# Performance work log

Hardware: AMD Instinct MI355X
Metric: run time of the kernel (lower is better)

Reference implementation:

```python
import jax, jax.numpy as jnp
import numpy as np

N_NODES = 50000
N_EDGES = 800000
D = 128


def setup_inputs() -> dict:
    key = jax.random.key(0)
    ks = jax.random.split(key, 5)
    x = jax.random.normal(ks[0], (N_NODES, D), dtype=jnp.float32)
    edge_index = jax.random.randint(ks[1], (2, N_EDGES), 0, N_NODES, dtype=jnp.int64)
    # GCNConv linear weight + bias, and the two DGCN parameters
    Wc = jax.random.normal(ks[2], (D, D), dtype=jnp.float32) / np.sqrt(D)
    bc = jnp.zeros((D,), dtype=jnp.float32)
    W0 = jax.random.normal(ks[3], (D, D), dtype=jnp.float32)
    Wt = jax.random.normal(ks[4], (D, D), dtype=jnp.float32)
    return {"x": x, "edge_index": edge_index, "Wc": Wc, "bc": bc, "W0": W0, "Wt": Wt}


def gcn_conv(x, edge_index, Wc, bc):
    # PyG GCNConv: add self-loops, symmetric normalization D^-1/2 (A+I) D^-1/2,
    # applied to x @ Wc, plus bias.
    n = x.shape[0]
    loops = jnp.arange(n, dtype=edge_index.dtype)
    src = jnp.concatenate([edge_index[0], loops])  # [E+N]
    dst = jnp.concatenate([edge_index[1], loops])
    ones = jnp.ones(src.shape[0], dtype=x.dtype)
    deg = jax.ops.segment_sum(ones, dst, num_segments=n)  # in-degree incl. self-loop
    dinv = jnp.where(deg > 0, jax.lax.rsqrt(deg), 0.0)
    norm = dinv[src] * dinv[dst]  # [E+N]
    xw = x @ Wc  # [N, D]
    msgs = xw[src] * norm[:, None]  # gather + scale  [E+N, D]
    agg = jax.ops.segment_sum(msgs, dst, num_segments=n)  # scatter-add  [N, D]
    return agg + bc


def reference(x, edge_index, Wc, bc, W0, Wt):
    h_neigh = gcn_conv(x, edge_index, Wc, bc)
    h_self = x @ W0
    h_change = (h_neigh - x) @ Wt
    return h_neigh + h_self + h_change
```

## Files before the change

### kernel.cpp

```cpp
#include <hip/hip_runtime.h>

#define N_NODES 50000
#define N_EDGES 800000
#define D 128
#define NB 196
#define CAPB 8192
#define P1_BLOCKS 256
#define EPB ((N_EDGES + P1_BLOCKS - 1) / P1_BLOCKS)
#define CAP 64

typedef __attribute__((ext_vector_type(8))) short short8;
typedef __attribute__((ext_vector_type(4))) float f32x4;

__device__ __forceinline__ unsigned short f2bf(float f) {
    unsigned int u = __builtin_bit_cast(unsigned int, f);
    u += 0x7FFFu + ((u >> 16) & 1u);
    return (unsigned short)(u >> 16);
}
__device__ __forceinline__ float bf2f(unsigned short h) {
    unsigned int u = ((unsigned int)h) << 16;
    return __builtin_bit_cast(float, u);
}

__global__ void k_init(int* __restrict__ gcur) {
    const int t = threadIdx.x;
    if (t < NB) gcur[t] = t * CAPB;
}

__global__ __launch_bounds__(256) void k_part1(const int* __restrict__ src,
                                               const int* __restrict__ dst,
                                               int* __restrict__ gcur,
                                               unsigned int* __restrict__ pbuf) {
    __shared__ unsigned int stage[NB][CAP + 1];
    __shared__ int scnt[NB];
    const int t = threadIdx.x;
    for (int i = t; i < NB; i += 256) scnt[i] = 0;
    __syncthreads();

    const long e0 = (long)blockIdx.x * EPB;
    const long e1 = (e0 + EPB < N_EDGES) ? e0 + EPB : N_EDGES;
    for (long e = e0 + t; e < e1; e += 256) {
        const int s = src[e];
        const int d = dst[e];
        const int b = d >> 8;
        const unsigned int p = ((unsigned int)(d & 255) << 16) | (unsigned int)s;
        const int slot = atomicAdd(&scnt[b], 1);
        if (slot < CAP) {
            stage[b][slot] = p;
        } else {
            const int pos = atomicAdd(&gcur[b], 1);
            pbuf[pos] = p;
        }
    }
    __syncthreads();
    if (t < NB) {
        const int n = (scnt[t] < CAP) ? scnt[t] : CAP;
        if (n > 0) {
            const int pos = atomicAdd(&gcur[t], n);
            for (int i = 0; i < n; ++i) pbuf[pos + i] = stage[t][i];
        }
    }
}

__global__ __launch_bounds__(256) void k_part2(const unsigned int* __restrict__ pbuf,
                                               const int* __restrict__ gcur,
                                               int* __restrict__ row_start,
                                               int* __restrict__ cnt,
                                               float* __restrict__ dinv,
                                               int* __restrict__ esrc) {
    __shared__ int lcnt[256];
    __shared__ int lcur[256];
    __shared__ int stmp[256];
    const int b = blockIdx.x;
    const int t = threadIdx.x;
    const int base = b * CAPB;
    const int n = gcur[b] - base;

    lcnt[t] = 0;
    __syncthreads();
    for (int i = t; i < n; i += 256) atomicAdd(&lcnt[pbuf[base + i] >> 16], 1);
    __syncthreads();

    const int c = lcnt[t];
    stmp[t] = c;
    __syncthreads();
    for (int off = 1; off < 256; off <<= 1) {
        int u = (t >= off) ? stmp[t - off] : 0;
        __syncthreads();
        stmp[t] += u;
        __syncthreads();
    }
    const int ls = base + stmp[t] - c;
    lcur[t] = ls;
    const int node = b * 256 + t;
    if (node < N_NODES) {
        row_start[node] = ls;
        cnt[node] = c;
        dinv[node] = rsqrtf((float)c + 1.0f);
    }
    __syncthreads();

    for (int i = t; i < n; i += 256) {
        const unsigned int p = pbuf[base + i];
        const int pos = atomicAdd(&lcur[p >> 16], 1);
        esrc[pos] = (int)(p & 0xFFFFu);
    }
}

__global__ __launch_bounds__(256) void k_wx(const float* __restrict__ Wc,
                                            const float* __restrict__ W0,
                                            const float* __restrict__ Wt,
                                            const float* __restrict__ bc,
                                            const float* __restrict__ x,
                                            const float* __restrict__ dinv,
                                            unsigned short* __restrict__ Wp,
                                            float* __restrict__ bv,
                                            unsigned short* __restrict__ xd,
                                            unsigned short* __restrict__ gx) {
    __shared__ float sWt[D * D];
    const int t = threadIdx.x;

    if (blockIdx.x < 17) {
        for (int i = t * 4; i < D * D; i += 256 * 4)
            *(float4*)(sWt + i) = *(const float4*)(Wt + i);
        __syncthreads();

        if (blockIdx.x == 16) {
            if (t < D) {
                float acc = bc[t];
#pragma unroll 16
                for (int k = 0; k < D; ++k) acc += bc[k] * sWt[k * D + t];
                bv[t] = acc;
            }
            return;
        }
        const int id = blockIdx.x * 256 + t;
        const int lane = id & 63;
        const int tile = (id >> 6) & 7;
        const int step = id >> 9;
        const int n = tile * 16 + (lane & 15);
        const int kbase = step * 32 + (lane >> 4) * 8;
        unsigned short v[8];
#pragma unroll
        for (int j = 0; j < 8; ++j) {
            const int k = kbase + j;
            float f;
            if (k < D) {
                f = Wc[k * D + n];
#pragma unroll 16
                for (int m = 0; m < D; ++m) f += Wc[k * D + m] * sWt[m * D + n];
            } else {
                f = W0[(k - D) * D + n] - sWt[(k - D) * D + n];
            }
            v[j] = f2bf(f);
        }
        *(uint4*)(Wp + (long)id * 8) = *(uint4*)v;
        return;
    }

    const int gid = (blockIdx.x - 17) * 256 + t;
    const int node = gid >> 4;
    const int c = gid & 15;
    const float di = dinv[node];
    const float4 a = ((const float4*)x)[(long)node * 32 + c * 2];
    const float4 b = ((const float4*)x)[(long)node * 32 + c * 2 + 1];
    const float f[8] = {a.x, a.y, a.z, a.w, b.x, b.y, b.z, b.w};
    unsigned short vd[8], vb[8];
#pragma unroll
    for (int j = 0; j < 8; ++j) {
        vd[j] = f2bf(di * f[j]);
        vb[j] = f2bf(f[j]);
    }
    *(uint4*)(xd + (long)node * 128 + c * 8) = *(uint4*)vd;
    *(uint4*)(gx + (long)node * 256 + 128 + c * 8) = *(uint4*)vb;
}

__global__ __launch_bounds__(256) void k_gather(const unsigned short* __restrict__ xd,
                                                const int* __restrict__ row_start,
                                                const int* __restrict__ cnt,
                                                const int* __restrict__ esrc,
                                                const float* __restrict__ dinv,
                                                unsigned short* __restrict__ gx) {
    const int node = blockIdx.x * 4 + (threadIdx.x >> 6);
    const int lane = threadIdx.x & 63;
    const int c = lane & 15;
    const int s = lane >> 4;
    const int begin = row_start[node];
    const int end = begin + cnt[node];

    float acc[8] = {};
    int i = begin + s;
    for (; i + 12 < end; i += 16) {
        const int a0 = esrc[i];
        const int a1 = esrc[i + 4];
        const int a2 = esrc[i + 8];
        const int a3 = esrc[i + 12];
        const short8 v0 = *(const short8*)(xd + (long)a0 * 128 + c * 8);
        const short8 v1 = *(const short8*)(xd + (long)a1 * 128 + c * 8);
        const short8 v2 = *(const short8*)(xd + (long)a2 * 128 + c * 8);
        const short8 v3 = *(const short8*)(xd + (long)a3 * 128 + c * 8);
#pragma unroll
        for (int j = 0; j < 8; ++j)
            acc[j] += (bf2f((unsigned short)v0[j]) + bf2f((unsigned short)v1[j])) +
                      (bf2f((unsigned short)v2[j]) + bf2f((unsigned short)v3[j]));
    }
    for (; i < end; i += 4) {
        const int a0 = esrc[i];
        const short8 v0 = *(const short8*)(xd + (long)a0 * 128 + c * 8);
#pragma unroll
        for (int j = 0; j < 8; ++j) acc[j] += bf2f((unsigned short)v0[j]);
    }

#pragma unroll
    for (int j = 0; j < 8; ++j) {
        acc[j] += __shfl_xor(acc[j], 16);
        acc[j] += __shfl_xor(acc[j], 32);
    }

    if (s == 0) {
        const float di = dinv[node];
        const short8 xs = *(const short8*)(xd + (long)node * 128 + c * 8);
        unsigned short o[8];
#pragma unroll
        for (int j = 0; j < 8; ++j)
            o[j] = f2bf(di * (acc[j] + bf2f((unsigned short)xs[j])));
        *(uint4*)(gx + (long)node * 256 + c * 8) = *(uint4*)o;
    }
}

__global__ __launch_bounds__(256) void k_mm(const unsigned short* __restrict__ gx,
                                            const unsigned short* __restrict__ Wp,
                                            const float* __restrict__ bv,
                                            float* __restrict__ out) {
    const int tid = threadIdx.x;
    const int wave = tid >> 6;
    const int lane = tid & 63;
    const int quad = lane >> 4;
    const int lr = lane & 15;
    const int row0 = blockIdx.x * 64 + wave * 16;

    int ar = row0 + lr;
    if (ar >= N_NODES) ar = N_NODES - 1;
    const unsigned short* aptr = gx + (long)ar * 256 + quad * 8;

    f32x4 acc[8] = {};

#pragma unroll
    for (int s = 0; s < 8; ++s) {
        const short8 a = *(const short8*)(aptr + s * 32);
#pragma unroll
        for (int t = 0; t < 8; ++t) {
            const short8 b = *(const short8*)(Wp + ((long)(s * 8 + t) * 64 + lane) * 8);
            acc[t] = __builtin_amdgcn_mfma_f32_16x16x32_bf16(a, b, acc[t], 0, 0, 0);
        }
    }

#pragma unroll
    for (int t = 0; t < 8; ++t) {
        const int col = t * 16 + lr;
        const float bvv = bv[col];
#pragma unroll
        for (int r = 0; r < 4; ++r) {
            const int row = row0 + quad * 4 + r;
            if (row < N_NODES) out[(long)row * D + col] = acc[t][r] + bvv;
        }
    }
}

extern "C" void kernel_launch(void* const* d_in, const int* in_sizes, int n_in,
                              void* d_out, int out_size, void* d_ws, size_t ws_size,
                              hipStream_t stream) {
    const float* x  = (const float*)d_in[0];
    const int*   ei = (const int*)d_in[1];
    const float* Wc = (const float*)d_in[2];
    const float* bc = (const float*)d_in[3];
    const float* W0 = (const float*)d_in[4];
    const float* Wt = (const float*)d_in[5];
    float* out = (float*)d_out;

    const int* src = ei;
    const int* dst = ei + N_EDGES;

    unsigned short* xd = (unsigned short*)d_ws;
    unsigned short* gx = xd + (size_t)N_NODES * 128;
    int*   cnt        = (int*)(gx + (size_t)N_NODES * 256);
    int*   row_start  = cnt + N_NODES;
    float* dinv       = (float*)(row_start + N_NODES);
    int*   esrc       = (int*)(dinv + N_NODES);
    unsigned int* pbuf = (unsigned int*)(esrc + (size_t)NB * CAPB);
    float* bv         = (float*)(pbuf + (size_t)NB * CAPB);
    unsigned short* Wp = (unsigned short*)(bv + D);
    int*   gcur       = (int*)(Wp + 256 * D);

    k_init<<<1, 256, 0, stream>>>(gcur);
    k_part1<<<P1_BLOCKS, 256, 0, stream>>>(src, dst, gcur, pbuf);
    k_part2<<<NB, 256, 0, stream>>>(pbuf, gcur, row_start, cnt, dinv, esrc);
    k_wx<<<17 + (N_NODES * 16) / 256, 256, 0, stream>>>(Wc, W0, Wt, bc, x, dinv,
                                                        Wp, bv, xd, gx);
    k_gather<<<N_NODES / 4, 256, 0, stream>>>(xd, row_start, cnt, esrc, dinv, gx);
    k_mm<<<(N_NODES + 63) / 64, 256, 0, stream>>>(gx, Wp, bv, out);
}
```

Before: 178.4 us.

## Fold weight precompute into partition kernel and x conversion into part2

```diff
diff --git a/kernel.cpp b/kernel.cpp
--- a/kernel.cpp
+++ b/kernel.cpp
@@ -30,11 +30,59 @@
 __global__ __launch_bounds__(256) void k_part1(const int* __restrict__ src,
                                                const int* __restrict__ dst,
                                                int* __restrict__ gcur,
-                                               unsigned int* __restrict__ pbuf) {
-    __shared__ unsigned int stage[NB][CAP + 1];
-    __shared__ int scnt[NB];
+                                               unsigned int* __restrict__ pbuf,
+                                               const float* __restrict__ Wc,
+                                               const float* __restrict__ W0,
+                                               const float* __restrict__ Wt,
+                                               const float* __restrict__ bc,
+                                               unsigned short* __restrict__ Wp,
+                                               float* __restrict__ bv) {
+    __shared__ union SM {
+        struct { unsigned int stage[NB][CAP + 1]; int scnt[NB]; } p;
+        float sWt[D * D];
+    } sm;
     const int t = threadIdx.x;
-    for (int i = t; i < NB; i += 256) scnt[i] = 0;
+
+    if (blockIdx.x >= P1_BLOCKS) {
+        const int wb = blockIdx.x - P1_BLOCKS;
+        for (int i = t * 4; i < D * D; i += 256 * 4)
+            *(float4*)(sm.sWt + i) = *(const float4*)(Wt + i);
+        __syncthreads();
+
+        if (wb == 16) {
+            if (t < D) {
+                float acc = bc[t];
+#pragma unroll 16
+                for (int k = 0; k < D; ++k) acc += bc[k] * sm.sWt[k * D + t];
+                bv[t] = acc;
+            }
+            return;
+        }
+        const int id = wb * 256 + t;
+        const int lane = id & 63;
+        const int tile = (id >> 6) & 7;
+        const int step = id >> 9;
+        const int n = tile * 16 + (lane & 15);
+        const int kbase = step * 32 + (lane >> 4) * 8;
+        unsigned short v[8];
+#pragma unroll
+        for (int j = 0; j < 8; ++j) {
+            const int k = kbase + j;
+            float f;
+            if (k < D) {
+                f = Wc[k * D + n];
+#pragma unroll 16
+                for (int m = 0; m < D; ++m) f += Wc[k * D + m] * sm.sWt[m * D + n];
+            } else {
+                f = W0[(k - D) * D + n] - sm.sWt[(k - D) * D + n];
+            }
+            v[j] = f2bf(f);
+        }
+        *(uint4*)(Wp + (long)id * 8) = *(uint4*)v;
+        return;
+    }
+
+    for (int i = t; i < NB; i += 256) sm.p.scnt[i] = 0;
     __syncthreads();
 
     const long e0 = (long)blockIdx.x * EPB;
@@ -44,9 +92,9 @@
         const int d = dst[e];
         const int b = d >> 8;
         const unsigned int p = ((unsigned int)(d & 255) << 16) | (unsigned int)s;
-        const int slot = atomicAdd(&scnt[b], 1);
+        const int slot = atomicAdd(&sm.p.scnt[b], 1);
         if (slot < CAP) {
-            stage[b][slot] = p;
+            sm.p.stage[b][slot] = p;
         } else {
             const int pos = atomicAdd(&gcur[b], 1);
             pbuf[pos] = p;
@@ -54,10 +102,10 @@
     }
     __syncthreads();
     if (t < NB) {
-        const int n = (scnt[t] < CAP) ? scnt[t] : CAP;
+        const int n = (sm.p.scnt[t] < CAP) ? sm.p.scnt[t] : CAP;
         if (n > 0) {
             const int pos = atomicAdd(&gcur[t], n);
-            for (int i = 0; i < n; ++i) pbuf[pos + i] = stage[t][i];
+            for (int i = 0; i < n; ++i) pbuf[pos + i] = sm.p.stage[t][i];
         }
     }
 }
@@ -67,10 +115,14 @@
                                                int* __restrict__ row_start,
                                                int* __restrict__ cnt,
                                                float* __restrict__ dinv,
-                                               int* __restrict__ esrc) {
+                                               int* __restrict__ esrc,
+                                               const float* __restrict__ x,
+                                               unsigned short* __restrict__ xd,
+                                               unsigned short* __restrict__ gx) {
     __shared__ int lcnt[256];
     __shared__ int lcur[256];
     __shared__ int stmp[256];
+    __shared__ float sdinv[256];
     const int b = blockIdx.x;
     const int t = threadIdx.x;
     const int base = b * CAPB;
@@ -92,11 +144,13 @@
     }
     const int ls = base + stmp[t] - c;
     lcur[t] = ls;
+    const float di = rsqrtf((float)c + 1.0f);
+    sdinv[t] = di;
     const int node = b * 256 + t;
     if (node < N_NODES) {
         row_start[node] = ls;
         cnt[node] = c;
-        dinv[node] = rsqrtf((float)c + 1.0f);
+        dinv[node] = di;
     }
     __syncthreads();
 
@@ -105,74 +159,27 @@
         const int pos = atomicAdd(&lcur[p >> 16], 1);
         esrc[pos] = (int)(p & 0xFFFFu);
     }
-}
-
-__global__ __launch_bounds__(256) void k_wx(const float* __restrict__ Wc,
-                                            const float* __restrict__ W0,
-                                            const float* __restrict__ Wt,
-                                            const float* __restrict__ bc,
-                                            const float* __restrict__ x,
-                                            const float* __restrict__ dinv,
-                                            unsigned short* __restrict__ Wp,
-                                            float* __restrict__ bv,
-                                            unsigned short* __restrict__ xd,
-                                            unsigned short* __restrict__ gx) {
-    __shared__ float sWt[D * D];
-    const int t = threadIdx.x;
-
-    if (blockIdx.x < 17) {
-        for (int i = t * 4; i < D * D; i += 256 * 4)
-            *(float4*)(sWt + i) = *(const float4*)(Wt + i);
-        __syncthreads();
-
-        if (blockIdx.x == 16) {
-            if (t < D) {
-                float acc = bc[t];
-#pragma unroll 16
-                for (int k = 0; k < D; ++k) acc += bc[k] * sWt[k * D + t];
-                bv[t] = acc;
+
+    const int cc = t & 15;
+    const int lr = t >> 4;
+    for (int it = 0; it < 16; ++it) {
+        const int nl = it * 16 + lr;
+        const int nd = b * 256 + nl;
+        if (nd < N_NODES) {
+            const float dv = sdinv[nl];
+            const float4 a = ((const float4*)x)[(long)nd * 32 + cc * 2];
+            const float4 bb = ((const float4*)x)[(long)nd * 32 + cc * 2 + 1];
+            const float f[8] = {a.x, a.y, a.z, a.w, bb.x, bb.y, bb.z, bb.w};
+            unsigned short vd[8], vb[8];
+#pragma unroll
+            for (int j = 0; j < 8; ++j) {
+                vd[j] = f2bf(dv * f[j]);
+                vb[j] = f2bf(f[j]);
             }
-            return;
-        }
-        const int id = blockIdx.x * 256 + t;
-        const int lane = id & 63;
-        const int tile = (id >> 6) & 7;
-        const int step = id >> 9;
-        const int n = tile * 16 + (lane & 15);
-        const int kbase = step * 32 + (lane >> 4) * 8;
-        unsigned short v[8];
-#pragma unroll
-        for (int j = 0; j < 8; ++j) {
-            const int k = kbase + j;
-            float f;
-            if (k < D) {
-                f = Wc[k * D + n];
-#pragma unroll 16
-                for (int m = 0; m < D; ++m) f += Wc[k * D + m] * sWt[m * D + n];
-            } else {
-                f = W0[(k - D) * D + n] - sWt[(k - D) * D + n];
-            }
-            v[j] = f2bf(f);
-        }
-        *(uint4*)(Wp + (long)id * 8) = *(uint4*)v;
-        return;
-    }
-
-    const int gid = (blockIdx.x - 17) * 256 + t;
-    const int node = gid >> 4;
-    const int c = gid & 15;
-    const float di = dinv[node];
-    const float4 a = ((const float4*)x)[(long)node * 32 + c * 2];
-    const float4 b = ((const float4*)x)[(long)node * 32 + c * 2 + 1];
-    const float f[8] = {a.x, a.y, a.z, a.w, b.x, b.y, b.z, b.w};
-    unsigned short vd[8], vb[8];
-#pragma unroll
-    for (int j = 0; j < 8; ++j) {
-        vd[j] = f2bf(di * f[j]);
-        vb[j] = f2bf(f[j]);
-    }
-    *(uint4*)(xd + (long)node * 128 + c * 8) = *(uint4*)vd;
-    *(uint4*)(gx + (long)node * 256 + 128 + c * 8) = *(uint4*)vb;
+            *(uint4*)(xd + (long)nd * 128 + cc * 8) = *(uint4*)vd;
+            *(uint4*)(gx + (long)nd * 256 + 128 + cc * 8) = *(uint4*)vb;
+        }
+    }
 }
 
 __global__ __launch_bounds__(256) void k_gather(const unsigned short* __restrict__ xd,
@@ -293,10 +300,10 @@
     int*   gcur       = (int*)(Wp + 256 * D);
 
     k_init<<<1, 256, 0, stream>>>(gcur);
-    k_part1<<<P1_BLOCKS, 256, 0, stream>>>(src, dst, gcur, pbuf);
-    k_part2<<<NB, 256, 0, stream>>>(pbuf, gcur, row_start, cnt, dinv, esrc);
-    k_wx<<<17 + (N_NODES * 16) / 256, 256, 0, stream>>>(Wc, W0, Wt, bc, x, dinv,
-                                                        Wp, bv, xd, gx);
+    k_part1<<<P1_BLOCKS + 17, 256, 0, stream>>>(src, dst, gcur, pbuf,
+                                                Wc, W0, Wt, bc, Wp, bv);
+    k_part2<<<NB, 256, 0, stream>>>(pbuf, gcur, row_start, cnt, dinv, esrc,
+                                    x, xd, gx);
     k_gather<<<N_NODES / 4, 256, 0, stream>>>(xd, row_start, cnt, esrc, dinv, gx);
     k_mm<<<(N_NODES + 63) / 64, 256, 0, stream>>>(gx, Wp, bv, out);
 }
```

Measured after the change: 186.7 us. 4.7% more time.

## Merge partition kernels into cooperative kernel and drop pre-scaled x copy

Applied to the files above, without the earlier changes.

```diff
diff --git a/kernel.cpp b/kernel.cpp
--- a/kernel.cpp
+++ b/kernel.cpp
@@ -1,4 +1,7 @@
 #include <hip/hip_runtime.h>
+#include <hip/hip_cooperative_groups.h>
+
+namespace cg = cooperative_groups;
 
 #define N_NODES 50000
 #define N_EDGES 800000
@@ -22,101 +25,14 @@
     return __builtin_bit_cast(float, u);
 }
 
-__global__ void k_init(int* __restrict__ gcur) {
-    const int t = threadIdx.x;
-    if (t < NB) gcur[t] = t * CAPB;
-}
-
-__global__ __launch_bounds__(256) void k_part1(const int* __restrict__ src,
-                                               const int* __restrict__ dst,
-                                               int* __restrict__ gcur,
-                                               unsigned int* __restrict__ pbuf) {
-    __shared__ unsigned int stage[NB][CAP + 1];
-    __shared__ int scnt[NB];
-    const int t = threadIdx.x;
-    for (int i = t; i < NB; i += 256) scnt[i] = 0;
-    __syncthreads();
-
-    const long e0 = (long)blockIdx.x * EPB;
-    const long e1 = (e0 + EPB < N_EDGES) ? e0 + EPB : N_EDGES;
-    for (long e = e0 + t; e < e1; e += 256) {
-        const int s = src[e];
-        const int d = dst[e];
-        const int b = d >> 8;
-        const unsigned int p = ((unsigned int)(d & 255) << 16) | (unsigned int)s;
-        const int slot = atomicAdd(&scnt[b], 1);
-        if (slot < CAP) {
-            stage[b][slot] = p;
-        } else {
-            const int pos = atomicAdd(&gcur[b], 1);
-            pbuf[pos] = p;
-        }
-    }
-    __syncthreads();
-    if (t < NB) {
-        const int n = (scnt[t] < CAP) ? scnt[t] : CAP;
-        if (n > 0) {
-            const int pos = atomicAdd(&gcur[t], n);
-            for (int i = 0; i < n; ++i) pbuf[pos + i] = stage[t][i];
-        }
-    }
-}
-
-__global__ __launch_bounds__(256) void k_part2(const unsigned int* __restrict__ pbuf,
-                                               const int* __restrict__ gcur,
-                                               int* __restrict__ row_start,
-                                               int* __restrict__ cnt,
-                                               float* __restrict__ dinv,
-                                               int* __restrict__ esrc) {
-    __shared__ int lcnt[256];
-    __shared__ int lcur[256];
-    __shared__ int stmp[256];
-    const int b = blockIdx.x;
-    const int t = threadIdx.x;
-    const int base = b * CAPB;
-    const int n = gcur[b] - base;
-
-    lcnt[t] = 0;
-    __syncthreads();
-    for (int i = t; i < n; i += 256) atomicAdd(&lcnt[pbuf[base + i] >> 16], 1);
-    __syncthreads();
-
-    const int c = lcnt[t];
-    stmp[t] = c;
-    __syncthreads();
-    for (int off = 1; off < 256; off <<= 1) {
-        int u = (t >= off) ? stmp[t - off] : 0;
-        __syncthreads();
-        stmp[t] += u;
-        __syncthreads();
-    }
-    const int ls = base + stmp[t] - c;
-    lcur[t] = ls;
-    const int node = b * 256 + t;
-    if (node < N_NODES) {
-        row_start[node] = ls;
-        cnt[node] = c;
-        dinv[node] = rsqrtf((float)c + 1.0f);
-    }
-    __syncthreads();
-
-    for (int i = t; i < n; i += 256) {
-        const unsigned int p = pbuf[base + i];
-        const int pos = atomicAdd(&lcur[p >> 16], 1);
-        esrc[pos] = (int)(p & 0xFFFFu);
-    }
-}
-
-__global__ __launch_bounds__(256) void k_wx(const float* __restrict__ Wc,
-                                            const float* __restrict__ W0,
-                                            const float* __restrict__ Wt,
-                                            const float* __restrict__ bc,
-                                            const float* __restrict__ x,
-                                            const float* __restrict__ dinv,
-                                            unsigned short* __restrict__ Wp,
-                                            float* __restrict__ bv,
-                                            unsigned short* __restrict__ xd,
-                                            unsigned short* __restrict__ gx) {
+__global__ __launch_bounds__(256) void k_pre(const float* __restrict__ Wc,
+                                             const float* __restrict__ W0,
+                                             const float* __restrict__ Wt,
+                                             const float* __restrict__ bc,
+                                             const float* __restrict__ x,
+                                             unsigned short* __restrict__ Wp,
+                                             float* __restrict__ bv,
+                                             unsigned short* __restrict__ xb) {
     __shared__ float sWt[D * D];
     const int t = threadIdx.x;
 
@@ -161,26 +77,104 @@
     const int gid = (blockIdx.x - 17) * 256 + t;
     const int node = gid >> 4;
     const int c = gid & 15;
-    const float di = dinv[node];
     const float4 a = ((const float4*)x)[(long)node * 32 + c * 2];
     const float4 b = ((const float4*)x)[(long)node * 32 + c * 2 + 1];
     const float f[8] = {a.x, a.y, a.z, a.w, b.x, b.y, b.z, b.w};
-    unsigned short vd[8], vb[8];
-#pragma unroll
-    for (int j = 0; j < 8; ++j) {
-        vd[j] = f2bf(di * f[j]);
-        vb[j] = f2bf(f[j]);
-    }
-    *(uint4*)(xd + (long)node * 128 + c * 8) = *(uint4*)vd;
-    *(uint4*)(gx + (long)node * 256 + 128 + c * 8) = *(uint4*)vb;
-}
-
-__global__ __launch_bounds__(256) void k_gather(const unsigned short* __restrict__ xd,
+    unsigned short vb[8];
+#pragma unroll
+    for (int j = 0; j < 8; ++j) vb[j] = f2bf(f[j]);
+    *(uint4*)(xb + (long)node * 128 + c * 8) = *(uint4*)vb;
+}
+
+__global__ __launch_bounds__(256) void k_part(const int* __restrict__ src,
+                                              const int* __restrict__ dst,
+                                              int* __restrict__ gcur,
+                                              unsigned int* __restrict__ pbuf,
+                                              int* __restrict__ row_start,
+                                              int* __restrict__ cnt,
+                                              float* __restrict__ dinv,
+                                              int* __restrict__ esrc) {
+    cg::grid_group grid = cg::this_grid();
+    __shared__ union SM {
+        struct { unsigned int stage[NB][CAP + 1]; int scnt[NB]; } p;
+        struct { int lcnt[256]; int lcur[256]; int stmp[256]; } q;
+    } sm;
+    const int t = threadIdx.x;
+    const int blk = blockIdx.x;
+
+    if (blk == 0 && t < NB) gcur[t] = 0;
+    grid.sync();
+
+    for (int i = t; i < NB; i += 256) sm.p.scnt[i] = 0;
+    __syncthreads();
+
+    const long e0 = (long)blk * EPB;
+    const long e1 = (e0 + EPB < N_EDGES) ? e0 + EPB : N_EDGES;
+    for (long e = e0 + t; e < e1; e += 256) {
+        const int s = src[e];
+        const int d = dst[e];
+        const int b = d >> 8;
+        const unsigned int p = ((unsigned int)(d & 255) << 16) | (unsigned int)s;
+        const int slot = atomicAdd(&sm.p.scnt[b], 1);
+        if (slot < CAP) {
+            sm.p.stage[b][slot] = p;
+        } else {
+            const int pos = atomicAdd(&gcur[b], 1);
+            pbuf[(long)b * CAPB + pos] = p;
+        }
+    }
+    __syncthreads();
+    if (t < NB) {
+        const int n = (sm.p.scnt[t] < CAP) ? sm.p.scnt[t] : CAP;
+        if (n > 0) {
+            const int pos = atomicAdd(&gcur[t], n);
+            for (int i = 0; i < n; ++i) pbuf[(long)t * CAPB + pos + i] = sm.p.stage[t][i];
+        }
+    }
+    grid.sync();
+
+    if (blk < NB) {
+        const int base = blk * CAPB;
+        const int n = gcur[blk];
+
+        sm.q.lcnt[t] = 0;
+        __syncthreads();
+        for (int i = t; i < n; i += 256) atomicAdd(&sm.q.lcnt[pbuf[base + i] >> 16], 1);
+        __syncthreads();
+
+        const int c = sm.q.lcnt[t];
+        sm.q.stmp[t] = c;
+        __syncthreads();
+        for (int off = 1; off < 256; off <<= 1) {
+            int u = (t >= off) ? sm.q.stmp[t - off] : 0;
+            __syncthreads();
+            sm.q.stmp[t] += u;
+            __syncthreads();
+        }
+        const int ls = base + sm.q.stmp[t] - c;
+        sm.q.lcur[t] = ls;
+        const int node = blk * 256 + t;
+        if (node < N_NODES) {
+            row_start[node] = ls;
+            cnt[node] = c;
+            dinv[node] = rsqrtf((float)c + 1.0f);
+        }
+        __syncthreads();
+
+        for (int i = t; i < n; i += 256) {
+            const unsigned int p = pbuf[base + i];
+            const int pos = atomicAdd(&sm.q.lcur[p >> 16], 1);
+            esrc[pos] = (int)(p & 0xFFFFu);
+        }
+    }
+}
+
+__global__ __launch_bounds__(256) void k_gather(const unsigned short* __restrict__ xb,
                                                 const int* __restrict__ row_start,
                                                 const int* __restrict__ cnt,
                                                 const int* __restrict__ esrc,
                                                 const float* __restrict__ dinv,
-                                                unsigned short* __restrict__ gx) {
+                                                unsigned short* __restrict__ g) {
     const int node = blockIdx.x * 4 + (threadIdx.x >> 6);
     const int lane = threadIdx.x & 63;
     const int c = lane & 15;
@@ -195,20 +189,25 @@
         const int a1 = esrc[i + 4];
         const int a2 = esrc[i + 8];
         const int a3 = esrc[i + 12];
-        const short8 v0 = *(const short8*)(xd + (long)a0 * 128 + c * 8);
-        const short8 v1 = *(const short8*)(xd + (long)a1 * 128 + c * 8);
-        const short8 v2 = *(const short8*)(xd + (long)a2 * 128 + c * 8);
-        const short8 v3 = *(const short8*)(xd + (long)a3 * 128 + c * 8);
+        const float d0 = dinv[a0];
+        const float d1 = dinv[a1];
+        const float d2 = dinv[a2];
+        const float d3 = dinv[a3];
+        const short8 v0 = *(const short8*)(xb + (long)a0 * 128 + c * 8);
+        const short8 v1 = *(const short8*)(xb + (long)a1 * 128 + c * 8);
+        const short8 v2 = *(const short8*)(xb + (long)a2 * 128 + c * 8);
+        const short8 v3 = *(const short8*)(xb + (long)a3 * 128 + c * 8);
 #pragma unroll
         for (int j = 0; j < 8; ++j)
-            acc[j] += (bf2f((unsigned short)v0[j]) + bf2f((unsigned short)v1[j])) +
-                      (bf2f((unsigned short)v2[j]) + bf2f((unsigned short)v3[j]));
+            acc[j] += (d0 * bf2f((unsigned short)v0[j]) + d1 * bf2f((unsigned short)v1[j])) +
+                      (d2 * bf2f((unsigned short)v2[j]) + d3 * bf2f((unsigned short)v3[j]));
     }
     for (; i < end; i += 4) {
         const int a0 = esrc[i];
-        const short8 v0 = *(const short8*)(xd + (long)a0 * 128 + c * 8);
-#pragma unroll
-        for (int j = 0; j < 8; ++j) acc[j] += bf2f((unsigned short)v0[j]);
+        const float d0 = dinv[a0];
+        const short8 v0 = *(const short8*)(xb + (long)a0 * 128 + c * 8);
+#pragma unroll
+        for (int j = 0; j < 8; ++j) acc[j] += d0 * bf2f((unsigned short)v0[j]);
     }
 
 #pragma unroll
@@ -219,16 +218,17 @@
 
     if (s == 0) {
         const float di = dinv[node];
-        const short8 xs = *(const short8*)(xd + (long)node * 128 + c * 8);
+        const short8 xs = *(const short8*)(xb + (long)node * 128 + c * 8);
         unsigned short o[8];
 #pragma unroll
         for (int j = 0; j < 8; ++j)
-            o[j] = f2bf(di * (acc[j] + bf2f((unsigned short)xs[j])));
-        *(uint4*)(gx + (long)node * 256 + c * 8) = *(uint4*)o;
-    }
-}
-
-__global__ __launch_bounds__(256) void k_mm(const unsigned short* __restrict__ gx,
+            o[j] = f2bf(di * (acc[j] + di * bf2f((unsigned short)xs[j])));
+        *(uint4*)(g + (long)node * 128 + c * 8) = *(uint4*)o;
+    }
+}
+
+__global__ __launch_bounds__(256) void k_mm(const unsigned short* __restrict__ g,
+                                            const unsigned short* __restrict__ xb,
                                             const unsigned short* __restrict__ Wp,
                                             const float* __restrict__ bv,
                                             float* __restrict__ out) {
@@ -241,13 +241,21 @@
 
     int ar = row0 + lr;
     if (ar >= N_NODES) ar = N_NODES - 1;
-    const unsigned short* aptr = gx + (long)ar * 256 + quad * 8;
 
     f32x4 acc[8] = {};
 
 #pragma unroll
-    for (int s = 0; s < 8; ++s) {
-        const short8 a = *(const short8*)(aptr + s * 32);
+    for (int s = 0; s < 4; ++s) {
+        const short8 a = *(const short8*)(g + (long)ar * 128 + s * 32 + quad * 8);
+#pragma unroll
+        for (int t = 0; t < 8; ++t) {
+            const short8 b = *(const short8*)(Wp + ((long)(s * 8 + t) * 64 + lane) * 8);
+            acc[t] = __builtin_amdgcn_mfma_f32_16x16x32_bf16(a, b, acc[t], 0, 0, 0);
+        }
+    }
+#pragma unroll
+    for (int s = 4; s < 8; ++s) {
+        const short8 a = *(const short8*)(xb + (long)ar * 128 + (s - 4) * 32 + quad * 8);
 #pragma unroll
         for (int t = 0; t < 8; ++t) {
             const short8 b = *(const short8*)(Wp + ((long)(s * 8 + t) * 64 + lane) * 8);
@@ -281,9 +289,9 @@
     const int* src = ei;
     const int* dst = ei + N_EDGES;
 
-    unsigned short* xd = (unsigned short*)d_ws;
-    unsigned short* gx = xd + (size_t)N_NODES * 128;
-    int*   cnt        = (int*)(gx + (size_t)N_NODES * 256);
+    unsigned short* xb = (unsigned short*)d_ws;
+    unsigned short* g  = xb + (size_t)N_NODES * 128;
+    int*   cnt        = (int*)(g + (size_t)N_NODES * 128);
     int*   row_start  = cnt + N_NODES;
     float* dinv       = (float*)(row_start + N_NODES);
     int*   esrc       = (int*)(dinv + N_NODES);
@@ -292,11 +300,13 @@
     unsigned short* Wp = (unsigned short*)(bv + D);
     int*   gcur       = (int*)(Wp + 256 * D);
 
-    k_init<<<1, 256, 0, stream>>>(gcur);
-    k_part1<<<P1_BLOCKS, 256, 0, stream>>>(src, dst, gcur, pbuf);
-    k_part2<<<NB, 256, 0, stream>>>(pbuf, gcur, row_start, cnt, dinv, esrc);
-    k_wx<<<17 + (N_NODES * 16) / 256, 256, 0, stream>>>(Wc, W0, Wt, bc, x, dinv,
-                                                        Wp, bv, xd, gx);
-    k_gather<<<N_NODES / 4, 256, 0, stream>>>(xd, row_start, cnt, esrc, dinv, gx);
-    k_mm<<<(N_NODES + 63) / 64, 256, 0, stream>>>(gx, Wp, bv, out);
-}
+    k_pre<<<17 + (N_NODES * 16) / 256, 256, 0, stream>>>(Wc, W0, Wt, bc, x, Wp, bv, xb);
+
+    void* pargs[] = {(void*)&src, (void*)&dst, (void*)&gcur, (void*)&pbuf,
+                     (void*)&row_start, (void*)&cnt, (void*)&dinv, (void*)&esrc};
+    hipLaunchCooperativeKernel((void*)k_part, dim3(P1_BLOCKS), dim3(256),
+                               pargs, 0, stream);
+
+    k_gather<<<N_NODES / 4, 256, 0, stream>>>(xb, row_start, cnt, esrc, dinv, g);
+    k_mm<<<(N_NODES + 63) / 64, 256, 0, stream>>>(g, xb, Wp, bv, out);
+}
```

After: 247.1 us. 38.5% more time.
